# Optimization experiments

Hardware: AMD Instinct MI355X
Metric: run time of the kernel (lower is better)

Reference implementation:

```python
import jax, jax.numpy as jnp
import numpy as np

B, S, H, T = 32, 512, 256, 48
START_IDX, STOP_IDX = 46, 47
NEG = -10000.0


def setup_inputs() -> dict:
    key = jax.random.key(0)
    k1, k2, k3, k4, k5 = jax.random.split(key, 5)
    lstm_features = jax.random.normal(k1, (B, S, H), dtype=jnp.float32)
    emission_w = jax.random.normal(k2, (H, T), dtype=jnp.float32) * 0.02
    emission_b = jnp.zeros((T,), dtype=jnp.float32)
    transitions = jax.random.normal(k3, (T, T), dtype=jnp.float32)
    transitions = transitions.at[:, START_IDX].set(NEG).at[STOP_IDX, :].set(NEG)
    lengths = jax.random.randint(k4, (B,), S // 2, S + 1, dtype=jnp.int32)
    tags = jax.random.randint(k5, (B, S), 0, START_IDX, dtype=jnp.int32)
    return {
        'lstm_features': lstm_features,
        'emission_w': emission_w,
        'emission_b': emission_b,
        'transitions': transitions,
        'lengths': lengths,
        'tags': tags,
    }


def _crf_scores(lstm_features, emission_w, emission_b, transitions):
    # emission: [B,S,T] at the 'to' tag; crf[b,s,i,j] = emission[b,s,j] + transitions[i,j]
    em = jnp.einsum('bsh,ht->bst', lstm_features, emission_w) + emission_b
    return em[:, :, None, :] + transitions[None, None, :, :]


def _forward_alg(crf_scores, transitions, lengths):
    # alpha[b,j] = log-sum-exp over paths ending at tag j
    alpha0 = jnp.full((B, T), NEG, dtype=crf_scores.dtype).at[:, START_IDX].set(0.0)

    def step(alpha, xs):
        crf_t, t = xs  # crf_t: [B,T,T]
        tag_var = crf_t + alpha[:, :, None]  # add score of 'from' tag
        new_alpha = jax.scipy.special.logsumexp(tag_var, axis=1)  # reduce over 'from'
        alpha = jnp.where((t < lengths)[:, None], new_alpha, alpha)
        return alpha, None

    xs = (jnp.swapaxes(crf_scores, 0, 1), jnp.arange(S, dtype=lengths.dtype))
    alpha, _ = jax.lax.scan(step, alpha0, xs)
    terminal = alpha + transitions[:, STOP_IDX][None, :]
    return jax.scipy.special.logsumexp(terminal, axis=1)  # [B]


def _gold_score(crf_scores, transitions, tags, lengths):
    # from_tags[t] = START for t=0 else tags[t-1]; to_tags[t] = tags[t]
    start_col = jnp.full((B, 1), START_IDX, dtype=tags.dtype)
    from_tags = jnp.concatenate([start_col, tags[:, :-1]], axis=1)  # [B,S]
    b_idx = jnp.arange(B)[:, None]
    s_idx = jnp.arange(S)[None, :]
    sel = crf_scores[b_idx, s_idx, from_tags, tags]  # [B,S]
    mask = (s_idx < lengths[:, None]).astype(sel.dtype)
    last_tag = jnp.take_along_axis(tags, (lengths - 1)[:, None], axis=1)[:, 0]
    return jnp.sum(sel * mask, axis=1) + transitions[last_tag, STOP_IDX]  # [B]


def reference(lstm_features, emission_w, emission_b, transitions, lengths, tags):
    crf_scores = _crf_scores(lstm_features, emission_w, emission_b, transitions)
    all_paths = _forward_alg(crf_scores, transitions, lengths)
    gold = _gold_score(crf_scores, transitions, tags, lengths)
    return all_paths - gold  # per-example NLL, shape [B]
```

## Files before the change

### kernel.cpp

```cpp
#include <hip/hip_runtime.h>
#include <math.h>

#define BB 32
#define SS 512
#define HH 256
#define TT 48
#define START_IDX 46
#define STOP_IDX 47

typedef __attribute__((ext_vector_type(8))) short short8;
typedef __attribute__((ext_vector_type(4))) float floatx4;

__device__ __forceinline__ float rfl(float x) {
    return __int_as_float(__builtin_amdgcn_readfirstlane(__float_as_int(x)));
}
__device__ __forceinline__ unsigned int bf16_rne(float x) {
    const unsigned int u = __float_as_uint(x);
    return (u + 0x7fffu + ((u >> 16) & 1u)) >> 16;
}
__device__ __forceinline__ float bf2f(unsigned short h) {
    return __uint_as_float(((unsigned int)h) << 16);
}

__global__ __launch_bounds__(256) void emission_kernel(
    const float* __restrict__ f, const float* __restrict__ w,
    const float* __restrict__ bias, const float* __restrict__ trans,
    unsigned short* __restrict__ exem, uint4* __restrict__ Ebuf)
{
    __shared__ __align__(16) char smem[50176];
    __shared__ float biaslds[TT];
    unsigned short* wb = (unsigned short*)smem;
    uint4* fragbuf = (uint4*)(smem + 25600);
    float* fl = (float*)smem;

    const int tid = threadIdx.x;

    if (blockIdx.x == 0 && tid < 64) {
        const int g = tid >> 4, cl = tid & 15;
#pragma unroll
        for (int kc = 0; kc < 2; ++kc)
#pragma unroll
            for (int nt = 0; nt < 3; ++nt) {
                unsigned int p[4];
#pragma unroll
                for (int h2 = 0; h2 < 4; ++h2) {
                    const int k = kc * 32 + g * 8 + 2 * h2;
                    const int n = nt * 16 + cl;
                    const float lo = (k     < TT) ? __expf(trans[k * TT + n])       : 0.f;
                    const float hi = (k + 1 < TT) ? __expf(trans[(k + 1) * TT + n]) : 0.f;
                    p[h2] = bf16_rne(lo) | (bf16_rne(hi) << 16);
                }
                Ebuf[(kc * 3 + nt) * 64 + tid] = make_uint4(p[0], p[1], p[2], p[3]);
            }
    }

    for (int idx = tid; idx < HH * TT; idx += 256) {
        const int r = idx / TT;
        const int c = idx - r * TT;
        wb[r * 50 + c] = (unsigned short)bf16_rne(w[idx]);
    }
    if (tid < TT) biaslds[tid] = bias[tid];
    __syncthreads();

    for (int idx = tid; idx < 24 * 64; idx += 256) {
        const int fb = idx >> 6;
        const int l  = idx & 63;
        const int kt = fb / 3;
        const int nt = fb - kt * 3;
        const int kbase = kt * 32 + (l >> 4) * 8;
        const int col   = nt * 16 + (l & 15);
        unsigned int p[4];
#pragma unroll
        for (int h2 = 0; h2 < 4; ++h2) {
            const unsigned int lo = wb[(kbase + 2 * h2)     * 50 + col];
            const unsigned int hi = wb[(kbase + 2 * h2 + 1) * 50 + col];
            p[h2] = lo | (hi << 16);
        }
        fragbuf[idx] = make_uint4(p[0], p[1], p[2], p[3]);
    }
    __syncthreads();

    const int lane = tid & 63, wv = tid >> 6, g = lane >> 4, cl = lane & 15;

    short8 Bf[24];
#pragma unroll
    for (int fb = 0; fb < 24; ++fb)
        Bf[fb] = __builtin_bit_cast(short8, fragbuf[fb * 64 + lane]);
    __syncthreads();

    const int row0 = blockIdx.x * 64;
    floatx4 acc0 = {0.f,0.f,0.f,0.f}, acc1 = {0.f,0.f,0.f,0.f}, acc2 = {0.f,0.f,0.f,0.f};

    const int lr = wv * 16 + cl;
#pragma unroll
    for (int h = 0; h < 2; ++h) {
#pragma unroll
        for (int it = 0; it < 8; ++it) {
            const int idx = tid + it * 256;
            const int r = idx >> 5, k4 = idx & 31;
            const float4 v = ((const float4*)f)[(size_t)(row0 + r) * 64 + h * 32 + k4];
            *(float4*)&fl[r * 132 + k4 * 4] = v;
        }
        __syncthreads();
#pragma unroll
        for (int kt = 0; kt < 4; ++kt) {
            const float4 v0 = *(const float4*)&fl[lr * 132 + kt * 32 + g * 8];
            const float4 v1 = *(const float4*)&fl[lr * 132 + kt * 32 + g * 8 + 4];
            const unsigned int a0 = bf16_rne(v0.x) | (bf16_rne(v0.y) << 16);
            const unsigned int a1 = bf16_rne(v0.z) | (bf16_rne(v0.w) << 16);
            const unsigned int a2 = bf16_rne(v1.x) | (bf16_rne(v1.y) << 16);
            const unsigned int a3 = bf16_rne(v1.z) | (bf16_rne(v1.w) << 16);
            const short8 Af = __builtin_bit_cast(short8, make_uint4(a0, a1, a2, a3));
            const int kg = h * 4 + kt;
            acc0 = __builtin_amdgcn_mfma_f32_16x16x32_bf16(Af, Bf[kg * 3 + 0], acc0, 0, 0, 0);
            acc1 = __builtin_amdgcn_mfma_f32_16x16x32_bf16(Af, Bf[kg * 3 + 1], acc1, 0, 0, 0);
            acc2 = __builtin_amdgcn_mfma_f32_16x16x32_bf16(Af, Bf[kg * 3 + 2], acc2, 0, 0, 0);
        }
        __syncthreads();
    }

    const int outrow0 = row0 + wv * 16 + g * 4;
    const int n = cl;
#pragma unroll
    for (int r = 0; r < 4; ++r) {
        unsigned short* e = exem + (size_t)(outrow0 + r) * TT;
        e[ 0 + n] = (unsigned short)bf16_rne(__expf(acc0[r] + biaslds[ 0 + n]));
        e[16 + n] = (unsigned short)bf16_rne(__expf(acc1[r] + biaslds[16 + n]));
        e[32 + n] = (unsigned short)bf16_rne(__expf(acc2[r] + biaslds[32 + n]));
    }
}

__global__ __launch_bounds__(192) void chunk_kernel(
    const unsigned short* __restrict__ exem,
    const uint4* __restrict__ Ebuf,
    const int*   __restrict__ lengths,
    unsigned short* __restrict__ Qs,
    float* __restrict__ Ls3)
{
    __shared__ __align__(8)  unsigned short ebuf[16 * TT];
    __shared__ __align__(16) unsigned short abuf[3][17 * 56];

    const int bc = blockIdx.x, b = bc >> 5, c = bc & 31;
    const int len = lengths[b];
    int nsteps = (len - 1) - (c << 4);
    if (nsteps <= 0) return;
    if (nsteps > 16) nsteps = 16;

    const int tid = threadIdx.x;
    const int rb = tid >> 6, l = tid & 63, g = l >> 4, cl = l & 15;

    {
        const unsigned int* src = (const unsigned int*)(exem + ((size_t)b * SS + (c << 4)) * TT);
        unsigned int* dst = (unsigned int*)ebuf;
        dst[tid] = src[tid];
        dst[tid + 192] = src[tid + 192];
    }

    uint4 Bf[2][3];
#pragma unroll
    for (int kc = 0; kc < 2; ++kc)
#pragma unroll
        for (int nt = 0; nt < 3; ++nt)
            Bf[kc][nt] = Ebuf[(kc * 3 + nt) * 64 + l];

    __syncthreads();

    floatx4 acc[3];
#pragma unroll
    for (int nt = 0; nt < 3; ++nt)
#pragma unroll
        for (int r = 0; r < 4; ++r)
            acc[nt][r] = (16 * rb + 4 * g + r == nt * 16 + cl) ? 1.f : 0.f;

    float ev[3];
#pragma unroll
    for (int nt = 0; nt < 3; ++nt) ev[nt] = bf2f(ebuf[nt * 16 + cl]);

    float Lrb = 0.f;
    unsigned short* aw = abuf[rb];

    for (int s = 0; s < nsteps; ++s) {
        float scale = 1.f;
        if (s == 8) {
            const float sig = rfl(acc[0][0]);
            Lrb = __logf(sig);
            scale = __builtin_amdgcn_rcpf(sig);
        }
        const float f0 = ev[0] * scale, f1 = ev[1] * scale, f2 = ev[2] * scale;
#pragma unroll
        for (int r = 0; r < 4; ++r) {
            const int rw = (4 * g + r) * 56;
            aw[rw +      cl] = (unsigned short)bf16_rne(acc[0][r] * f0);
            aw[rw + 16 + cl] = (unsigned short)bf16_rne(acc[1][r] * f1);
            aw[rw + 32 + cl] = (unsigned short)bf16_rne(acc[2][r] * f2);
        }
        if (s + 1 < nsteps) {
#pragma unroll
            for (int nt = 0; nt < 3; ++nt)
                ev[nt] = bf2f(ebuf[(s + 1) * TT + nt * 16 + cl]);
        }
        uint4 a0 = *(const uint4*)&aw[cl * 56 + g * 8];
        uint4 a1 = *(const uint4*)&aw[cl * 56 + 32 + g * 8];
        if (g >= 2) a1 = make_uint4(0, 0, 0, 0);
        const floatx4 z = {0.f, 0.f, 0.f, 0.f};
#pragma unroll
        for (int nt = 0; nt < 3; ++nt) {
            floatx4 d = __builtin_amdgcn_mfma_f32_16x16x32_bf16(
                __builtin_bit_cast(short8, a0), __builtin_bit_cast(short8, Bf[0][nt]), z, 0, 0, 0);
            d = __builtin_amdgcn_mfma_f32_16x16x32_bf16(
                __builtin_bit_cast(short8, a1), __builtin_bit_cast(short8, Bf[1][nt]), d, 0, 0, 0);
            acc[nt] = d;
        }
    }

    unsigned short* qb = Qs + (size_t)bc * (TT * 64);
#pragma unroll
    for (int nt = 0; nt < 3; ++nt) {
        const unsigned int lo = bf16_rne(acc[nt][0]) | (bf16_rne(acc[nt][1]) << 16);
        const unsigned int hi = bf16_rne(acc[nt][2]) | (bf16_rne(acc[nt][3]) << 16);
        *(uint2*)&qb[(nt * 16 + cl) * 64 + 16 * rb + 4 * g] = make_uint2(lo, hi);
    }
    if (l == 0) Ls3[bc * 3 + rb] = Lrb;
}

__global__ __launch_bounds__(256) void finalize_kernel(
    const unsigned short* __restrict__ exem,
    const float* __restrict__ trans,
    const int*   __restrict__ lengths,
    const int*   __restrict__ tags,
    const unsigned short* __restrict__ Qs,
    const float* __restrict__ Ls3,
    float* __restrict__ out)
{
    __shared__ float tlds[TT * TT];
    __shared__ __align__(16) unsigned short Mlds[4][TT * 72];
    __shared__ __align__(16) unsigned short aw4[4][TT * 56 + 16];
    __shared__ float Lsl[96], fal[96];
    __shared__ float Lw[4], golds[4];
    __shared__ __align__(16) unsigned short vlds[64];

    const int tid = threadIdx.x, b = blockIdx.x;
    const int wv = tid >> 6, l = tid & 63, g = l >> 4, cl = l & 15;

    for (int idx = tid; idx < TT * TT; idx += 256) tlds[idx] = trans[idx];

    const int len = lengths[b];
    const int nc = (len - 1 + 15) >> 4;

    if (tid < 96) Lsl[tid] = (tid < nc * 3) ? Ls3[b * 96 + tid] : 0.f;
    __syncthreads();

    if (tid < 96) fal[tid] = __expf(Lsl[tid] - Lsl[(tid / 3) * 3]);

    float gold = 0.f;
    for (int s = tid; s < len; s += 256) {
        const int tag  = tags[b * SS + s];
        const int from = (s == 0) ? START_IDX : tags[b * SS + s - 1];
        gold += __logf(bf2f(exem[((size_t)b * SS + s) * TT + tag])) + tlds[from * TT + tag];
    }
    gold += __shfl_xor(gold, 32); gold += __shfl_xor(gold, 16); gold += __shfl_xor(gold, 8);
    gold += __shfl_xor(gold, 4);  gold += __shfl_xor(gold, 2);  gold += __shfl_xor(gold, 1);
    if (l == 0) golds[wv] = gold;
    __syncthreads();

    const int K  = (nc + 3) >> 2;
    const int c0 = wv * K;
    const int c1 = (c0 + K < nc) ? (c0 + K) : nc;

    floatx4 M[3][3];
#pragma unroll
    for (int mt = 0; mt < 3; ++mt)
#pragma unroll
        for (int nt = 0; nt < 3; ++nt)
#pragma unroll
            for (int r = 0; r < 4; ++r)
                M[mt][nt][r] = (16 * mt + 4 * g + r == 16 * nt + cl) ? 1.f : 0.f;

    float inv = 1.f, Lacc = 0.f;
    unsigned short* aw = aw4[wv];
    const unsigned short* qbase = Qs + (size_t)(b * 32) * (TT * 64);

    uint4 pB0[3], pB1[3];
    if (c0 < c1) {
#pragma unroll
        for (int nt = 0; nt < 3; ++nt) {
            pB0[nt] = *(const uint4*)&qbase[(size_t)c0 * TT * 64 + (nt * 16 + cl) * 64 + g * 8];
            pB1[nt] = *(const uint4*)&qbase[(size_t)c0 * TT * 64 + (nt * 16 + cl) * 64 + 32 + g * 8];
        }
    }

    for (int c = c0; c < c1; ++c) {
        uint4 B0[3], B1[3];
#pragma unroll
        for (int nt = 0; nt < 3; ++nt) {
            B0[nt] = pB0[nt];
            B1[nt] = pB1[nt];
            if (g >= 2) B1[nt] = make_uint4(0, 0, 0, 0);
        }
        const int cn = (c + 1 < c1) ? c + 1 : c;
#pragma unroll
        for (int nt = 0; nt < 3; ++nt) {
            pB0[nt] = *(const uint4*)&qbase[(size_t)cn * TT * 64 + (nt * 16 + cl) * 64 + g * 8];
            pB1[nt] = *(const uint4*)&qbase[(size_t)cn * TT * 64 + (nt * 16 + cl) * 64 + 32 + g * 8];
        }

        const float f0 = inv * fal[c * 3 + 0];
        const float f1 = inv * fal[c * 3 + 1];
        const float f2 = inv * fal[c * 3 + 2];
        Lacc += Lsl[c * 3];

#pragma unroll
        for (int mt = 0; mt < 3; ++mt)
#pragma unroll
            for (int r = 0; r < 4; ++r) {
                const int rw = (16 * mt + 4 * g + r) * 56;
                aw[rw +      cl] = (unsigned short)bf16_rne(M[mt][0][r] * f0);
                aw[rw + 16 + cl] = (unsigned short)bf16_rne(M[mt][1][r] * f1);
                aw[rw + 32 + cl] = (unsigned short)bf16_rne(M[mt][2][r] * f2);
            }

        uint4 A0[3], A1[3];
#pragma unroll
        for (int mt = 0; mt < 3; ++mt) {
            A0[mt] = *(const uint4*)&aw[(16 * mt + cl) * 56 + g * 8];
            A1[mt] = *(const uint4*)&aw[(16 * mt + cl) * 56 + 32 + g * 8];
            if (g >= 2) A1[mt] = make_uint4(0, 0, 0, 0);
        }

        const floatx4 z = {0.f, 0.f, 0.f, 0.f};
#pragma unroll
        for (int mt = 0; mt < 3; ++mt)
#pragma unroll
            for (int nt = 0; nt < 3; ++nt) {
                floatx4 d = __builtin_amdgcn_mfma_f32_16x16x32_bf16(
                    __builtin_bit_cast(short8, A0[mt]), __builtin_bit_cast(short8, B0[nt]), z, 0, 0, 0);
                d = __builtin_amdgcn_mfma_f32_16x16x32_bf16(
                    __builtin_bit_cast(short8, A1[mt]), __builtin_bit_cast(short8, B1[nt]), d, 0, 0, 0);
                M[mt][nt] = d;
            }
        const float sig = rfl(M[0][0][0]);
        inv = __builtin_amdgcn_rcpf(sig);
        Lacc += __logf(sig);
    }

#pragma unroll
    for (int mt = 0; mt < 3; ++mt)
#pragma unroll
        for (int nt = 0; nt < 3; ++nt) {
            const unsigned int lo = bf16_rne(M[mt][nt][0] * inv) | (bf16_rne(M[mt][nt][1] * inv) << 16);
            const unsigned int hi = bf16_rne(M[mt][nt][2] * inv) | (bf16_rne(M[mt][nt][3] * inv) << 16);
            *(uint2*)&Mlds[wv][(nt * 16 + cl) * 72 + 16 * mt + 4 * g] = make_uint2(lo, hi);
        }
    if (l == 0) Lw[wv] = Lacc;
    __syncthreads();

    if (wv == 0) {
        const float vj = (l < TT) ? __expf(tlds[START_IDX * TT + l]) : 0.f;
        vlds[l] = (unsigned short)bf16_rne(vj);

        float L = 0.f, cinv = 1.f;
        floatx4 accn[3];

        for (int w = 0; w < 4; ++w) {
            uint4 B0[3], B1[3];
#pragma unroll
            for (int nt = 0; nt < 3; ++nt) {
                B0[nt] = *(const uint4*)&Mlds[w][(nt * 16 + cl) * 72 + g * 8];
                B1[nt] = *(const uint4*)&Mlds[w][(nt * 16 + cl) * 72 + 32 + g * 8];
                if (g >= 2) B1[nt] = make_uint4(0, 0, 0, 0);
            }
            const uint4 A0 = *(const uint4*)&vlds[g * 8];
            const uint4 A1 = *(const uint4*)&vlds[32 + g * 8];

            const floatx4 z = {0.f, 0.f, 0.f, 0.f};
#pragma unroll
            for (int nt = 0; nt < 3; ++nt) {
                floatx4 d = __builtin_amdgcn_mfma_f32_16x16x32_bf16(
                    __builtin_bit_cast(short8, A0), __builtin_bit_cast(short8, B0[nt]), z, 0, 0, 0);
                d = __builtin_amdgcn_mfma_f32_16x16x32_bf16(
                    __builtin_bit_cast(short8, A1), __builtin_bit_cast(short8, B1[nt]), d, 0, 0, 0);
                accn[nt] = d;
            }
            const float sig = rfl(accn[0][0]);
            cinv = __builtin_amdgcn_rcpf(sig);
            L += __logf(sig) + Lw[w];
            if (w < 3 && l < 16) {
                vlds[ 0 + l] = (unsigned short)bf16_rne(accn[0][0] * cinv);
                vlds[16 + l] = (unsigned short)bf16_rne(accn[1][0] * cinv);
                vlds[32 + l] = (unsigned short)bf16_rne(accn[2][0] * cinv);
            }
        }

        float term = 0.f;
        if (l < 16) {
            const size_t erow = ((size_t)b * SS + (len - 1)) * TT;
#pragma unroll
            for (int nt = 0; nt < 3; ++nt) {
                const int col = nt * 16 + l;
                term += accn[nt][0] * cinv * bf2f(exem[erow + col])
                        * __expf(tlds[col * TT + STOP_IDX]);
            }
        }
        term += __shfl_xor(term, 32); term += __shfl_xor(term, 16); term += __shfl_xor(term, 8);
        term += __shfl_xor(term, 4);  term += __shfl_xor(term, 2);  term += __shfl_xor(term, 1);

        if (l == 0) {
            const float all_paths = __logf(term) + L;
            const int last = tags[b * SS + len - 1];
            out[b] = all_paths
                     - (golds[0] + golds[1] + golds[2] + golds[3] + tlds[last * TT + STOP_IDX]);
        }
    }
}

extern "C" void kernel_launch(void* const* d_in, const int* in_sizes, int n_in,
                              void* d_out, int out_size, void* d_ws, size_t ws_size,
                              hipStream_t stream) {
    const float* f       = (const float*)d_in[0];
    const float* w       = (const float*)d_in[1];
    const float* bias    = (const float*)d_in[2];
    const float* trans   = (const float*)d_in[3];
    const int*   lengths = (const int*)d_in[4];
    const int*   tags    = (const int*)d_in[5];
    float*       out     = (float*)d_out;

    char* ws = (char*)d_ws;
    unsigned short* exem = (unsigned short*)ws;
    unsigned short* Qs   = (unsigned short*)(ws + 1572864);
    float*          Lsc  = (float*)(ws + 7864320);
    uint4*          Ebuf = (uint4*)(ws + 7876608);

    emission_kernel<<<(BB * SS) / 64, 256, 0, stream>>>(f, w, bias, trans, exem, Ebuf);
    chunk_kernel<<<BB * 32, 192, 0, stream>>>(exem, Ebuf, lengths, Qs, Lsc);
    finalize_kernel<<<BB, 256, 0, stream>>>(exem, trans, lengths, tags, Qs, Lsc, out);
}
```

Baseline: 109.5 us.

## Fuse emission GEMM, chunk scan and finalize into one kernel with last-block reduction

Replaces the three-kernel pipeline with a small prep kernel that packs W and exp(transitions) into MFMA fragments, plus one fused kernel per (batch, chunk). Each block computes its own 16-row emission tile, accumulates the gold score with an atomic, runs the chunk matrix-product scan, and the last-arriving block per batch (atomic counter) does the finalize combine. This removes kernel launch gaps, the full emission round trip, and a separate finalize grid. The cost is atomics and threadfences, finalize work now serialized into one 192-thread block split across 3 waves, and a counter reset that relies on prep_kernel running first.

```diff
diff --git a/kernel.cpp b/kernel.cpp
--- a/kernel.cpp
+++ b/kernel.cpp
@@ -22,250 +22,229 @@
     return __uint_as_float(((unsigned int)h) << 16);
 }
 
-__global__ __launch_bounds__(256) void emission_kernel(
-    const float* __restrict__ f, const float* __restrict__ w,
-    const float* __restrict__ bias, const float* __restrict__ trans,
-    unsigned short* __restrict__ exem, uint4* __restrict__ Ebuf)
+__global__ __launch_bounds__(256) void prep_kernel(
+    const float* __restrict__ w, const float* __restrict__ trans,
+    uint4* __restrict__ Ebuf, uint4* __restrict__ Wbuf,
+    unsigned int* __restrict__ cnt, float* __restrict__ goldb)
 {
-    __shared__ __align__(16) char smem[50176];
-    __shared__ float biaslds[TT];
-    unsigned short* wb = (unsigned short*)smem;
-    uint4* fragbuf = (uint4*)(smem + 25600);
-    float* fl = (float*)smem;
-
-    const int tid = threadIdx.x;
-
-    if (blockIdx.x == 0 && tid < 64) {
-        const int g = tid >> 4, cl = tid & 15;
-#pragma unroll
-        for (int kc = 0; kc < 2; ++kc)
-#pragma unroll
-            for (int nt = 0; nt < 3; ++nt) {
-                unsigned int p[4];
-#pragma unroll
-                for (int h2 = 0; h2 < 4; ++h2) {
-                    const int k = kc * 32 + g * 8 + 2 * h2;
-                    const int n = nt * 16 + cl;
-                    const float lo = (k     < TT) ? __expf(trans[k * TT + n])       : 0.f;
-                    const float hi = (k + 1 < TT) ? __expf(trans[(k + 1) * TT + n]) : 0.f;
-                    p[h2] = bf16_rne(lo) | (bf16_rne(hi) << 16);
+    __shared__ unsigned short wb[64 * 50];
+    const int tid = threadIdx.x, blk = blockIdx.x;
+
+    if (blk == 4) {
+        if (tid < 32) { cnt[tid] = 0u; goldb[tid] = 0.f; }
+        if (tid < 64) {
+            const int g = tid >> 4, cl = tid & 15;
+#pragma unroll
+            for (int kc = 0; kc < 2; ++kc)
+#pragma unroll
+                for (int nt = 0; nt < 3; ++nt) {
+                    unsigned int p[4];
+#pragma unroll
+                    for (int h2 = 0; h2 < 4; ++h2) {
+                        const int k = kc * 32 + g * 8 + 2 * h2;
+                        const int n = nt * 16 + cl;
+                        const float lo = (k     < TT) ? __expf(trans[k * TT + n])       : 0.f;
+                        const float hi = (k + 1 < TT) ? __expf(trans[(k + 1) * TT + n]) : 0.f;
+                        p[h2] = bf16_rne(lo) | (bf16_rne(hi) << 16);
+                    }
+                    Ebuf[(kc * 3 + nt) * 64 + tid] = make_uint4(p[0], p[1], p[2], p[3]);
                 }
-                Ebuf[(kc * 3 + nt) * 64 + tid] = make_uint4(p[0], p[1], p[2], p[3]);
-            }
-    }
-
-    for (int idx = tid; idx < HH * TT; idx += 256) {
-        const int r = idx / TT;
-        const int c = idx - r * TT;
-        wb[r * 50 + c] = (unsigned short)bf16_rne(w[idx]);
-    }
-    if (tid < TT) biaslds[tid] = bias[tid];
-    __syncthreads();
-
-    for (int idx = tid; idx < 24 * 64; idx += 256) {
-        const int fb = idx >> 6;
-        const int l  = idx & 63;
-        const int kt = fb / 3;
-        const int nt = fb - kt * 3;
-        const int kbase = kt * 32 + (l >> 4) * 8;
-        const int col   = nt * 16 + (l & 15);
+        }
+        return;
+    }
+
+    const int kt0 = blk * 2;
+    const int R0  = kt0 * 32;
+    for (int i = tid; i < 768; i += 256) {
+        const float4 v = ((const float4*)w)[R0 * 12 + i];
+        const int lr = i / 12, c4 = (i - lr * 12) * 4;
+        unsigned short* d = &wb[lr * 50 + c4];
+        d[0] = (unsigned short)bf16_rne(v.x);
+        d[1] = (unsigned short)bf16_rne(v.y);
+        d[2] = (unsigned short)bf16_rne(v.z);
+        d[3] = (unsigned short)bf16_rne(v.w);
+    }
+    __syncthreads();
+    for (int idx = tid; idx < 384; idx += 256) {
+        const int fbl = idx >> 6, l = idx & 63;
+        const int ktl = fbl / 3, nt = fbl - ktl * 3;
+        const int kb  = ktl * 32 + (l >> 4) * 8;
+        const int col = nt * 16 + (l & 15);
         unsigned int p[4];
 #pragma unroll
         for (int h2 = 0; h2 < 4; ++h2) {
-            const unsigned int lo = wb[(kbase + 2 * h2)     * 50 + col];
-            const unsigned int hi = wb[(kbase + 2 * h2 + 1) * 50 + col];
+            const unsigned int lo = wb[(kb + 2 * h2)     * 50 + col];
+            const unsigned int hi = wb[(kb + 2 * h2 + 1) * 50 + col];
             p[h2] = lo | (hi << 16);
         }
-        fragbuf[idx] = make_uint4(p[0], p[1], p[2], p[3]);
-    }
-    __syncthreads();
-
-    const int lane = tid & 63, wv = tid >> 6, g = lane >> 4, cl = lane & 15;
-
-    short8 Bf[24];
-#pragma unroll
-    for (int fb = 0; fb < 24; ++fb)
-        Bf[fb] = __builtin_bit_cast(short8, fragbuf[fb * 64 + lane]);
-    __syncthreads();
-
-    const int row0 = blockIdx.x * 64;
-    floatx4 acc0 = {0.f,0.f,0.f,0.f}, acc1 = {0.f,0.f,0.f,0.f}, acc2 = {0.f,0.f,0.f,0.f};
-
-    const int lr = wv * 16 + cl;
-#pragma unroll
-    for (int h = 0; h < 2; ++h) {
-#pragma unroll
-        for (int it = 0; it < 8; ++it) {
-            const int idx = tid + it * 256;
-            const int r = idx >> 5, k4 = idx & 31;
-            const float4 v = ((const float4*)f)[(size_t)(row0 + r) * 64 + h * 32 + k4];
-            *(float4*)&fl[r * 132 + k4 * 4] = v;
-        }
-        __syncthreads();
-#pragma unroll
-        for (int kt = 0; kt < 4; ++kt) {
-            const float4 v0 = *(const float4*)&fl[lr * 132 + kt * 32 + g * 8];
-            const float4 v1 = *(const float4*)&fl[lr * 132 + kt * 32 + g * 8 + 4];
-            const unsigned int a0 = bf16_rne(v0.x) | (bf16_rne(v0.y) << 16);
-            const unsigned int a1 = bf16_rne(v0.z) | (bf16_rne(v0.w) << 16);
-            const unsigned int a2 = bf16_rne(v1.x) | (bf16_rne(v1.y) << 16);
-            const unsigned int a3 = bf16_rne(v1.z) | (bf16_rne(v1.w) << 16);
-            const short8 Af = __builtin_bit_cast(short8, make_uint4(a0, a1, a2, a3));
-            const int kg = h * 4 + kt;
-            acc0 = __builtin_amdgcn_mfma_f32_16x16x32_bf16(Af, Bf[kg * 3 + 0], acc0, 0, 0, 0);
-            acc1 = __builtin_amdgcn_mfma_f32_16x16x32_bf16(Af, Bf[kg * 3 + 1], acc1, 0, 0, 0);
-            acc2 = __builtin_amdgcn_mfma_f32_16x16x32_bf16(Af, Bf[kg * 3 + 2], acc2, 0, 0, 0);
-        }
-        __syncthreads();
-    }
-
-    const int outrow0 = row0 + wv * 16 + g * 4;
-    const int n = cl;
-#pragma unroll
-    for (int r = 0; r < 4; ++r) {
-        unsigned short* e = exem + (size_t)(outrow0 + r) * TT;
-        e[ 0 + n] = (unsigned short)bf16_rne(__expf(acc0[r] + biaslds[ 0 + n]));
-        e[16 + n] = (unsigned short)bf16_rne(__expf(acc1[r] + biaslds[16 + n]));
-        e[32 + n] = (unsigned short)bf16_rne(__expf(acc2[r] + biaslds[32 + n]));
-    }
-}
-
-__global__ __launch_bounds__(192) void chunk_kernel(
-    const unsigned short* __restrict__ exem,
-    const uint4* __restrict__ Ebuf,
-    const int*   __restrict__ lengths,
-    unsigned short* __restrict__ Qs,
-    float* __restrict__ Ls3)
+        Wbuf[((kt0 + ktl) * 3 + nt) * 64 + l] = make_uint4(p[0], p[1], p[2], p[3]);
+    }
+}
+
+__global__ __launch_bounds__(192, 3) void fused_kernel(
+    const float* __restrict__ f, const float* __restrict__ bias,
+    const float* __restrict__ trans, const int* __restrict__ lengths,
+    const int* __restrict__ tags,
+    unsigned short* __restrict__ exem, unsigned short* __restrict__ Qs,
+    float* __restrict__ Ls3, const uint4* __restrict__ Ebuf,
+    const uint4* __restrict__ Wbuf, unsigned int* __restrict__ cnt,
+    float* __restrict__ goldb, float* __restrict__ out)
 {
-    __shared__ __align__(8)  unsigned short ebuf[16 * TT];
+    __shared__ __align__(16) unsigned short ebuf[16 * TT];
     __shared__ __align__(16) unsigned short abuf[3][17 * 56];
+    __shared__ __align__(16) unsigned short pool_us[3 * 2704];
+    __shared__ float Lsl[96], fal[96], Lw[3];
+    __shared__ __align__(16) unsigned short vlds[64];
+    __shared__ int flag;
 
     const int bc = blockIdx.x, b = bc >> 5, c = bc & 31;
     const int len = lengths[b];
-    int nsteps = (len - 1) - (c << 4);
-    if (nsteps <= 0) return;
-    if (nsteps > 16) nsteps = 16;
-
-    const int tid = threadIdx.x;
-    const int rb = tid >> 6, l = tid & 63, g = l >> 4, cl = l & 15;
-
-    {
-        const unsigned int* src = (const unsigned int*)(exem + ((size_t)b * SS + (c << 4)) * TT);
-        unsigned int* dst = (unsigned int*)ebuf;
-        dst[tid] = src[tid];
-        dst[tid + 192] = src[tid + 192];
-    }
-
-    uint4 Bf[2][3];
-#pragma unroll
-    for (int kc = 0; kc < 2; ++kc)
+    const int tid = threadIdx.x, wv = tid >> 6, l = tid & 63, g = l >> 4, cl = l & 15;
+    const int base16 = c << 4;
+
+    const int nraw = (len - 1) - base16;
+    const bool active = (nraw >= 0);
+    int nsteps = (nraw > 16) ? 16 : nraw;
+
+    float* plds = (float*)pool_us;
+
+    if (active) {
+        const float* frow = f + ((size_t)b * SS + base16 + cl) * HH + g * 8;
+        float4 fv[8][2];
+#pragma unroll
+        for (int kt = 0; kt < 8; ++kt) {
+            fv[kt][0] = *(const float4*)(frow + kt * 32);
+            fv[kt][1] = *(const float4*)(frow + kt * 32 + 4);
+        }
+        uint4 wf[8];
+#pragma unroll
+        for (int kt = 0; kt < 8; ++kt) wf[kt] = Wbuf[(kt * 3 + wv) * 64 + l];
+
+        floatx4 acc = {0.f, 0.f, 0.f, 0.f};
+#pragma unroll
+        for (int kt = 0; kt < 8; ++kt) {
+            const unsigned int a0 = bf16_rne(fv[kt][0].x) | (bf16_rne(fv[kt][0].y) << 16);
+            const unsigned int a1 = bf16_rne(fv[kt][0].z) | (bf16_rne(fv[kt][0].w) << 16);
+            const unsigned int a2 = bf16_rne(fv[kt][1].x) | (bf16_rne(fv[kt][1].y) << 16);
+            const unsigned int a3 = bf16_rne(fv[kt][1].z) | (bf16_rne(fv[kt][1].w) << 16);
+            const short8 Af = __builtin_bit_cast(short8, make_uint4(a0, a1, a2, a3));
+            acc = __builtin_amdgcn_mfma_f32_16x16x32_bf16(
+                Af, __builtin_bit_cast(short8, wf[kt]), acc, 0, 0, 0);
+        }
+        const float bcol = bias[wv * 16 + cl];
+#pragma unroll
+        for (int r = 0; r < 4; ++r) {
+            const int row = 4 * g + r, col = wv * 16 + cl;
+            const float el = acc[r] + bcol;
+            plds[row * 48 + col] = el;
+            ebuf[row * TT + col] = (unsigned short)bf16_rne(__expf(el));
+        }
+    }
+    __syncthreads();
+
+    if (active) {
+        if (tid < 96)
+            ((uint4*)(exem + ((size_t)b * SS + base16) * TT))[tid] = ((const uint4*)ebuf)[tid];
+
+        if (wv == 0) {
+            float gp = 0.f;
+            if (l < 16) {
+                const int s = base16 + l;
+                if (s < len) {
+                    const int tag  = tags[b * SS + s];
+                    const int from = (s == 0) ? START_IDX : tags[b * SS + s - 1];
+                    gp = plds[l * 48 + tag] + trans[from * TT + tag];
+                }
+            }
+            gp += __shfl_xor(gp, 8); gp += __shfl_xor(gp, 4);
+            gp += __shfl_xor(gp, 2); gp += __shfl_xor(gp, 1);
+            if (l == 0) atomicAdd(&goldb[b], gp);
+        }
+    }
+
+    if (nsteps > 0) {
+        uint4 Bf[2][3];
+#pragma unroll
+        for (int kc = 0; kc < 2; ++kc)
+#pragma unroll
+            for (int nt = 0; nt < 3; ++nt)
+                Bf[kc][nt] = Ebuf[(kc * 3 + nt) * 64 + l];
+
+        floatx4 acc[3];
 #pragma unroll
         for (int nt = 0; nt < 3; ++nt)
-            Bf[kc][nt] = Ebuf[(kc * 3 + nt) * 64 + l];
-
-    __syncthreads();
-
-    floatx4 acc[3];
-#pragma unroll
-    for (int nt = 0; nt < 3; ++nt)
-#pragma unroll
-        for (int r = 0; r < 4; ++r)
-            acc[nt][r] = (16 * rb + 4 * g + r == nt * 16 + cl) ? 1.f : 0.f;
-
-    float ev[3];
-#pragma unroll
-    for (int nt = 0; nt < 3; ++nt) ev[nt] = bf2f(ebuf[nt * 16 + cl]);
-
-    float Lrb = 0.f;
-    unsigned short* aw = abuf[rb];
-
-    for (int s = 0; s < nsteps; ++s) {
-        float scale = 1.f;
-        if (s == 8) {
-            const float sig = rfl(acc[0][0]);
-            Lrb = __logf(sig);
-            scale = __builtin_amdgcn_rcpf(sig);
-        }
-        const float f0 = ev[0] * scale, f1 = ev[1] * scale, f2 = ev[2] * scale;
-#pragma unroll
-        for (int r = 0; r < 4; ++r) {
-            const int rw = (4 * g + r) * 56;
-            aw[rw +      cl] = (unsigned short)bf16_rne(acc[0][r] * f0);
-            aw[rw + 16 + cl] = (unsigned short)bf16_rne(acc[1][r] * f1);
-            aw[rw + 32 + cl] = (unsigned short)bf16_rne(acc[2][r] * f2);
-        }
-        if (s + 1 < nsteps) {
-#pragma unroll
-            for (int nt = 0; nt < 3; ++nt)
-                ev[nt] = bf2f(ebuf[(s + 1) * TT + nt * 16 + cl]);
-        }
-        uint4 a0 = *(const uint4*)&aw[cl * 56 + g * 8];
-        uint4 a1 = *(const uint4*)&aw[cl * 56 + 32 + g * 8];
-        if (g >= 2) a1 = make_uint4(0, 0, 0, 0);
-        const floatx4 z = {0.f, 0.f, 0.f, 0.f};
+#pragma unroll
+            for (int r = 0; r < 4; ++r)
+                acc[nt][r] = (16 * wv + 4 * g + r == nt * 16 + cl) ? 1.f : 0.f;
+
+        float ev[3];
+#pragma unroll
+        for (int nt = 0; nt < 3; ++nt) ev[nt] = bf2f(ebuf[nt * 16 + cl]);
+
+        float Lrb = 0.f;
+        unsigned short* aw = abuf[wv];
+
+        for (int s = 0; s < nsteps; ++s) {
+            float scale = 1.f;
+            if (s == 8) {
+                const float sig = rfl(acc[0][0]);
+                Lrb = __logf(sig);
+                scale = __builtin_amdgcn_rcpf(sig);
+            }
+            const float f0 = ev[0] * scale, f1 = ev[1] * scale, f2 = ev[2] * scale;
+#pragma unroll
+            for (int r = 0; r < 4; ++r) {
+                const int rw = (4 * g + r) * 56;
+                aw[rw +      cl] = (unsigned short)bf16_rne(acc[0][r] * f0);
+                aw[rw + 16 + cl] = (unsigned short)bf16_rne(acc[1][r] * f1);
+                aw[rw + 32 + cl] = (unsigned short)bf16_rne(acc[2][r] * f2);
+            }
+            if (s + 1 < nsteps) {
+#pragma unroll
+                for (int nt = 0; nt < 3; ++nt)
+                    ev[nt] = bf2f(ebuf[(s + 1) * TT + nt * 16 + cl]);
+            }
+            uint4 a0 = *(const uint4*)&aw[cl * 56 + g * 8];
+            uint4 a1 = *(const uint4*)&aw[cl * 56 + 32 + g * 8];
+            if (g >= 2) a1 = make_uint4(0, 0, 0, 0);
+            const floatx4 z = {0.f, 0.f, 0.f, 0.f};
+#pragma unroll
+            for (int nt = 0; nt < 3; ++nt) {
+                floatx4 d = __builtin_amdgcn_mfma_f32_16x16x32_bf16(
+                    __builtin_bit_cast(short8, a0), __builtin_bit_cast(short8, Bf[0][nt]), z, 0, 0, 0);
+                d = __builtin_amdgcn_mfma_f32_16x16x32_bf16(
+                    __builtin_bit_cast(short8, a1), __builtin_bit_cast(short8, Bf[1][nt]), d, 0, 0, 0);
+                acc[nt] = d;
+            }
+        }
+
+        unsigned short* qb = Qs + (size_t)bc * (TT * 64);
 #pragma unroll
         for (int nt = 0; nt < 3; ++nt) {
-            floatx4 d = __builtin_amdgcn_mfma_f32_16x16x32_bf16(
-                __builtin_bit_cast(short8, a0), __builtin_bit_cast(short8, Bf[0][nt]), z, 0, 0, 0);
-            d = __builtin_amdgcn_mfma_f32_16x16x32_bf16(
-                __builtin_bit_cast(short8, a1), __builtin_bit_cast(short8, Bf[1][nt]), d, 0, 0, 0);
-            acc[nt] = d;
-        }
-    }
-
-    unsigned short* qb = Qs + (size_t)bc * (TT * 64);
-#pragma unroll
-    for (int nt = 0; nt < 3; ++nt) {
-        const unsigned int lo = bf16_rne(acc[nt][0]) | (bf16_rne(acc[nt][1]) << 16);
-        const unsigned int hi = bf16_rne(acc[nt][2]) | (bf16_rne(acc[nt][3]) << 16);
-        *(uint2*)&qb[(nt * 16 + cl) * 64 + 16 * rb + 4 * g] = make_uint2(lo, hi);
-    }
-    if (l == 0) Ls3[bc * 3 + rb] = Lrb;
-}
-
-__global__ __launch_bounds__(256) void finalize_kernel(
-    const unsigned short* __restrict__ exem,
-    const float* __restrict__ trans,
-    const int*   __restrict__ lengths,
-    const int*   __restrict__ tags,
-    const unsigned short* __restrict__ Qs,
-    const float* __restrict__ Ls3,
-    float* __restrict__ out)
-{
-    __shared__ float tlds[TT * TT];
-    __shared__ __align__(16) unsigned short Mlds[4][TT * 72];
-    __shared__ __align__(16) unsigned short aw4[4][TT * 56 + 16];
-    __shared__ float Lsl[96], fal[96];
-    __shared__ float Lw[4], golds[4];
-    __shared__ __align__(16) unsigned short vlds[64];
-
-    const int tid = threadIdx.x, b = blockIdx.x;
-    const int wv = tid >> 6, l = tid & 63, g = l >> 4, cl = l & 15;
-
-    for (int idx = tid; idx < TT * TT; idx += 256) tlds[idx] = trans[idx];
-
-    const int len = lengths[b];
+            const unsigned int lo = bf16_rne(acc[nt][0]) | (bf16_rne(acc[nt][1]) << 16);
+            const unsigned int hi = bf16_rne(acc[nt][2]) | (bf16_rne(acc[nt][3]) << 16);
+            *(uint2*)&qb[(nt * 16 + cl) * 64 + 16 * wv + 4 * g] = make_uint2(lo, hi);
+        }
+        if (l == 0) Ls3[bc * 3 + wv] = Lrb;
+    }
+
+    __threadfence();
+    __syncthreads();
+    if (tid == 0) flag = (atomicAdd(&cnt[b], 1u) == 31u) ? 1 : 0;
+    __syncthreads();
+    if (!flag) return;
+    __threadfence();
+
     const int nc = (len - 1 + 15) >> 4;
-
     if (tid < 96) Lsl[tid] = (tid < nc * 3) ? Ls3[b * 96 + tid] : 0.f;
     __syncthreads();
-
     if (tid < 96) fal[tid] = __expf(Lsl[tid] - Lsl[(tid / 3) * 3]);
-
-    float gold = 0.f;
-    for (int s = tid; s < len; s += 256) {
-        const int tag  = tags[b * SS + s];
-        const int from = (s == 0) ? START_IDX : tags[b * SS + s - 1];
-        gold += __logf(bf2f(exem[((size_t)b * SS + s) * TT + tag])) + tlds[from * TT + tag];
-    }
-    gold += __shfl_xor(gold, 32); gold += __shfl_xor(gold, 16); gold += __shfl_xor(gold, 8);
-    gold += __shfl_xor(gold, 4);  gold += __shfl_xor(gold, 2);  gold += __shfl_xor(gold, 1);
-    if (l == 0) golds[wv] = gold;
-    __syncthreads();
-
-    const int K  = (nc + 3) >> 2;
-    const int c0 = wv * K;
-    const int c1 = (c0 + K < nc) ? (c0 + K) : nc;
+    __syncthreads();
+
+    unsigned short* paw = pool_us + wv * 2704;
+    const int K3 = (nc + 2) / 3;
+    const int c0 = wv * K3;
+    const int c1 = (c0 + K3 < nc) ? c0 + K3 : nc;
 
     floatx4 M[3][3];
 #pragma unroll
@@ -277,19 +256,16 @@
                 M[mt][nt][r] = (16 * mt + 4 * g + r == 16 * nt + cl) ? 1.f : 0.f;
 
     float inv = 1.f, Lacc = 0.f;
-    unsigned short* aw = aw4[wv];
     const unsigned short* qbase = Qs + (size_t)(b * 32) * (TT * 64);
 
     uint4 pB0[3], pB1[3];
-    if (c0 < c1) {
-#pragma unroll
-        for (int nt = 0; nt < 3; ++nt) {
-            pB0[nt] = *(const uint4*)&qbase[(size_t)c0 * TT * 64 + (nt * 16 + cl) * 64 + g * 8];
-            pB1[nt] = *(const uint4*)&qbase[(size_t)c0 * TT * 64 + (nt * 16 + cl) * 64 + 32 + g * 8];
-        }
-    }
-
-    for (int c = c0; c < c1; ++c) {
+#pragma unroll
+    for (int nt = 0; nt < 3; ++nt) {
+        pB0[nt] = *(const uint4*)&qbase[(size_t)c0 * TT * 64 + (nt * 16 + cl) * 64 + g * 8];
+        pB1[nt] = *(const uint4*)&qbase[(size_t)c0 * TT * 64 + (nt * 16 + cl) * 64 + 32 + g * 8];
+    }
+
+    for (int c2 = c0; c2 < c1; ++c2) {
         uint4 B0[3], B1[3];
 #pragma unroll
         for (int nt = 0; nt < 3; ++nt) {
@@ -297,33 +273,33 @@
             B1[nt] = pB1[nt];
             if (g >= 2) B1[nt] = make_uint4(0, 0, 0, 0);
         }
-        const int cn = (c + 1 < c1) ? c + 1 : c;
+        const int cn = (c2 + 1 < c1) ? c2 + 1 : c2;
 #pragma unroll
         for (int nt = 0; nt < 3; ++nt) {
             pB0[nt] = *(const uint4*)&qbase[(size_t)cn * TT * 64 + (nt * 16 + cl) * 64 + g * 8];
             pB1[nt] = *(const uint4*)&qbase[(size_t)cn * TT * 64 + (nt * 16 + cl) * 64 + 32 + g * 8];
         }
 
-        const float f0 = inv * fal[c * 3 + 0];
-        const float f1 = inv * fal[c * 3 + 1];
-        const float f2 = inv * fal[c * 3 + 2];
-        Lacc += Lsl[c * 3];
+        const float f0 = inv * fal[c2 * 3 + 0];
+        const float f1 = inv * fal[c2 * 3 + 1];
+        const float f2 = inv * fal[c2 * 3 + 2];
+        Lacc += Lsl[c2 * 3];
 
 #pragma unroll
         for (int mt = 0; mt < 3; ++mt)
 #pragma unroll
             for (int r = 0; r < 4; ++r) {
                 const int rw = (16 * mt + 4 * g + r) * 56;
-                aw[rw +      cl] = (unsigned short)bf16_rne(M[mt][0][r] * f0);
-                aw[rw + 16 + cl] = (unsigned short)bf16_rne(M[mt][1][r] * f1);
-                aw[rw + 32 + cl] = (unsigned short)bf16_rne(M[mt][2][r] * f2);
+                paw[rw +      cl] = (unsigned short)bf16_rne(M[mt][0][r] * f0);
+                paw[rw + 16 + cl] = (unsigned short)bf16_rne(M[mt][1][r] * f1);
+                paw[rw + 32 + cl] = (unsigned short)bf16_rne(M[mt][2][r] * f2);
             }
 
         uint4 A0[3], A1[3];
 #pragma unroll
         for (int mt = 0; mt < 3; ++mt) {
-            A0[mt] = *(const uint4*)&aw[(16 * mt + cl) * 56 + g * 8];
-            A1[mt] = *(const uint4*)&aw[(16 * mt + cl) * 56 + 32 + g * 8];
+            A0[mt] = *(const uint4*)&paw[(16 * mt + cl) * 56 + g * 8];
+            A1[mt] = *(const uint4*)&paw[(16 * mt + cl) * 56 + 32 + g * 8];
             if (g >= 2) A1[mt] = make_uint4(0, 0, 0, 0);
         }
 
@@ -349,24 +325,25 @@
         for (int nt = 0; nt < 3; ++nt) {
             const unsigned int lo = bf16_rne(M[mt][nt][0] * inv) | (bf16_rne(M[mt][nt][1] * inv) << 16);
             const unsigned int hi = bf16_rne(M[mt][nt][2] * inv) | (bf16_rne(M[mt][nt][3] * inv) << 16);
-            *(uint2*)&Mlds[wv][(nt * 16 + cl) * 72 + 16 * mt + 4 * g] = make_uint2(lo, hi);
+            *(uint2*)&paw[(nt * 16 + cl) * 56 + 16 * mt + 4 * g] = make_uint2(lo, hi);
         }
     if (l == 0) Lw[wv] = Lacc;
     __syncthreads();
 
     if (wv == 0) {
-        const float vj = (l < TT) ? __expf(tlds[START_IDX * TT + l]) : 0.f;
+        const float vj = (l < TT) ? __expf(trans[START_IDX * TT + l]) : 0.f;
         vlds[l] = (unsigned short)bf16_rne(vj);
 
         float L = 0.f, cinv = 1.f;
         floatx4 accn[3];
 
-        for (int w = 0; w < 4; ++w) {
+        for (int w3 = 0; w3 < 3; ++w3) {
+            const unsigned short* pw = pool_us + w3 * 2704;
             uint4 B0[3], B1[3];
 #pragma unroll
             for (int nt = 0; nt < 3; ++nt) {
-                B0[nt] = *(const uint4*)&Mlds[w][(nt * 16 + cl) * 72 + g * 8];
-                B1[nt] = *(const uint4*)&Mlds[w][(nt * 16 + cl) * 72 + 32 + g * 8];
+                B0[nt] = *(const uint4*)&pw[(nt * 16 + cl) * 56 + g * 8];
+                B1[nt] = *(const uint4*)&pw[(nt * 16 + cl) * 56 + 32 + g * 8];
                 if (g >= 2) B1[nt] = make_uint4(0, 0, 0, 0);
             }
             const uint4 A0 = *(const uint4*)&vlds[g * 8];
@@ -383,8 +360,8 @@
             }
             const float sig = rfl(accn[0][0]);
             cinv = __builtin_amdgcn_rcpf(sig);
-            L += __logf(sig) + Lw[w];
-            if (w < 3 && l < 16) {
+            L += __logf(sig) + Lw[w3];
+            if (w3 < 2 && l < 16) {
                 vlds[ 0 + l] = (unsigned short)bf16_rne(accn[0][0] * cinv);
                 vlds[16 + l] = (unsigned short)bf16_rne(accn[1][0] * cinv);
                 vlds[32 + l] = (unsigned short)bf16_rne(accn[2][0] * cinv);
@@ -398,7 +375,7 @@
             for (int nt = 0; nt < 3; ++nt) {
                 const int col = nt * 16 + l;
                 term += accn[nt][0] * cinv * bf2f(exem[erow + col])
-                        * __expf(tlds[col * TT + STOP_IDX]);
+                        * __expf(trans[col * TT + STOP_IDX]);
             }
         }
         term += __shfl_xor(term, 32); term += __shfl_xor(term, 16); term += __shfl_xor(term, 8);
@@ -407,8 +384,7 @@
         if (l == 0) {
             const float all_paths = __logf(term) + L;
             const int last = tags[b * SS + len - 1];
-            out[b] = all_paths
-                     - (golds[0] + golds[1] + golds[2] + golds[3] + tlds[last * TT + STOP_IDX]);
+            out[b] = all_paths - (goldb[b] + trans[last * TT + STOP_IDX]);
         }
     }
 }
@@ -429,8 +405,11 @@
     unsigned short* Qs   = (unsigned short*)(ws + 1572864);
     float*          Lsc  = (float*)(ws + 7864320);
     uint4*          Ebuf = (uint4*)(ws + 7876608);
-
-    emission_kernel<<<(BB * SS) / 64, 256, 0, stream>>>(f, w, bias, trans, exem, Ebuf);
-    chunk_kernel<<<BB * 32, 192, 0, stream>>>(exem, Ebuf, lengths, Qs, Lsc);
-    finalize_kernel<<<BB, 256, 0, stream>>>(exem, trans, lengths, tags, Qs, Lsc, out);
-}
+    uint4*          Wbuf = (uint4*)(ws + 7882752);
+    unsigned int*   cnt  = (unsigned int*)(ws + 7907328);
+    float*          goldb= (float*)(ws + 7907456);
+
+    prep_kernel<<<5, 256, 0, stream>>>(w, trans, Ebuf, Wbuf, cnt, goldb);
+    fused_kernel<<<BB * 32, 192, 0, stream>>>(f, bias, trans, lengths, tags,
+                                              exem, Qs, Lsc, Ebuf, Wbuf, cnt, goldb, out);
+}
```

Result: slower. 207.0 us (+89.0%).
